# Kernel tuning notes

Hardware: AMD Instinct MI355X
Metric: run time of the kernel (lower is better)

## Reference

```python
import jax, jax.numpy as jnp
import numpy as np

B, T, D = 4096, 200, 64
H = 32  # hidden units of score MLP
NEG_INF = jnp.float32(-2**32 + 1)


def setup_inputs() -> dict:
    key = jax.random.key(0)
    k1, k2, k3, k4, k5 = jax.random.split(key, 5)
    query = jax.random.normal(k1, (B, 1, D), dtype=jnp.float32)
    keys = jax.random.normal(k2, (B, T, D), dtype=jnp.float32)
    mask = jax.random.randint(k3, (B, T), 0, 2) > 0
    mask = mask.at[:, 0].set(True)  # ensure at least one valid key per row
    # Glorot-normal-ish init for the tiny score MLP
    W1 = jax.random.normal(k4, (3 * D, H), dtype=jnp.float32) * jnp.sqrt(2.0 / (3 * D + H))
    b1 = jnp.zeros((H,), dtype=jnp.float32)
    W2 = jax.random.normal(k5, (H, 1), dtype=jnp.float32) * jnp.sqrt(2.0 / (H + 1))
    b2 = jnp.zeros((1,), dtype=jnp.float32)
    return {"query": query, "keys": keys, "mask": mask,
            "W1": W1, "b1": b1, "W2": W2, "b2": b2}


def reference(query, keys, mask, W1, b1, W2, b2):
    b, t, d = keys.shape
    q = jnp.broadcast_to(query, (b, t, d))            # tile query over seq
    att_in = jnp.concatenate([q, keys, q - keys], axis=-1)   # [B,T,3D]
    h = jax.nn.sigmoid(att_in @ W1 + b1)              # [B,T,H]
    score = (h @ W2 + b2)[..., 0]                     # [B,T]
    score = jnp.where(mask, score, NEG_INF)
    w = jax.nn.softmax(score, axis=-1)                # [B,T]
    out = jnp.einsum('bt,btd->bd', w, keys)           # weighted key sum
    return out[:, None, :]                            # [B,1,D]
```

## Files before the change

kernel.cpp:

```cpp
#include <hip/hip_runtime.h>
#include <hip/hip_bf16.h>


#define B 4096
#define T 200
#define D 64
#define H 32
#define LOG2E 1.44269504088896340736f
#define SOFF 16.0f
#define NTILE 13

typedef __attribute__((ext_vector_type(8))) short short8;
typedef __attribute__((ext_vector_type(4))) float f32x4;


__global__ __launch_bounds__(256) void prep_kernel(
        const float* __restrict__ W1,
        float*       __restrict__ ws)
{
    int n = blockIdx.x * 256 + threadIdx.x;
    if (blockIdx.x < 8) {
        int k = n >> 5;
        int j = n & 31;
        ws[n] = W1[k * H + j] + W1[(128 + k) * H + j];
    } else {
        int m = n - 2048;
        int e  = m & 7;
        int l  = (m >> 3) & 63;
        int fs = m >> 9;
        int ntile = fs >> 1, kstep = fs & 1;
        int k = kstep * 32 + (l >> 4) * 8 + e;
        int j = ntile * 16 + (l & 15);
        float v = W1[(64 + k) * H + j] - W1[(128 + k) * H + j];
        __hip_bfloat16 hv = __float2bfloat16(v);
        reinterpret_cast<unsigned short*>(ws + 2048)[m] =
            __builtin_bit_cast(unsigned short, hv);
    }
}

__device__ __forceinline__ unsigned short bf16u(float x) {
    __hip_bfloat16 h = __float2bfloat16(x);
    return __builtin_bit_cast(unsigned short, h);
}

__global__ __launch_bounds__(256) void attn_pool_kernel(
        const float* __restrict__ keys,
        const int*   __restrict__ mask,
        const unsigned short* __restrict__ wkf,
        const float* __restrict__ wsum,
        const float* __restrict__ b1,
        const float* __restrict__ W2,
        const float* __restrict__ query,
        float*       __restrict__ out)
{
    __shared__ float qsh[4][64];
    __shared__ float part[4][68];

    const int tid  = threadIdx.x;
    const int wv   = tid >> 6;
    const int lane = tid & 63;
    const int quad = lane >> 4;
    const int l15  = lane & 15;

    const int b    = blockIdx.x * 2 + (wv >> 1);
    const int half = wv & 1;

    qsh[wv][lane] = query[(size_t)b * D + lane];
    const int jq = lane & 31;
    const int kh = lane >> 5;
    float qac0 = kh ? 0.0f : b1[jq];
    float qac1 = 0.0f;
    #pragma unroll
    for (int k0 = 0; k0 < 32; k0 += 2) {
        int k = kh * 32 + k0;
        qac0 = fmaf(qsh[wv][k],     wsum[k * H + jq],       qac0);
        qac1 = fmaf(qsh[wv][k + 1], wsum[(k + 1) * H + jq], qac1);
    }
    float qac = qac0 + qac1;
    qac += __shfl_xor(qac, 32, 64);
    const float qa0 = __shfl(qac, l15, 64);
    const float qa1 = __shfl(qac, 16 + l15, 64);

    const short8* wf = reinterpret_cast<const short8*>(wkf);
    short8 bf0 = wf[0 * 64 + lane];
    short8 bf1 = wf[1 * 64 + lane];
    short8 bf2 = wf[2 * 64 + lane];
    short8 bf3 = wf[3 * 64 + lane];
    const float w20 = W2[l15];
    const float w21 = W2[16 + l15];

    const float4* krow = reinterpret_cast<const float4*>(keys + (size_t)b * (T * D));
    const int*    mrow = mask + (size_t)b * T;
    const int ib = quad * 2;

    float acc[16];
    #pragma unroll
    for (int j = 0; j < 16; ++j) acc[j] = 0.0f;
    float dacc = 0.0f;

    const int t0  = half * 7;
    const int ntl = half ? 6 : 7;

    float4 kA0 = krow[(t0 * 16 + l15) * 16 + ib + 0];
    float4 kA1 = krow[(t0 * 16 + l15) * 16 + ib + 1];
    float4 kA2 = krow[(t0 * 16 + l15) * 16 + 8 + ib + 0];
    float4 kA3 = krow[(t0 * 16 + l15) * 16 + 8 + ib + 1];
    int    mA  = mrow[t0 * 16 + l15];

    #pragma unroll 1
    for (int it = 0; it < ntl; ++it) {
        const int tile = t0 + it;
        float4 kB0 = kA0, kB1 = kA1, kB2 = kA2, kB3 = kA3;
        int    mB  = mA;
        if (it + 1 < ntl) {
            int tn  = (tile + 1) * 16 + l15;
            int trn = (tn < T) ? tn : (T - 1);
            kB0 = krow[trn * 16 + ib + 0];
            kB1 = krow[trn * 16 + ib + 1];
            kB2 = krow[trn * 16 + 8 + ib + 0];
            kB3 = krow[trn * 16 + 8 + ib + 1];
            mB  = mrow[trn];
        }

        short8 a0, a1;
        a0[0] = (short)bf16u(kA0.x); a0[1] = (short)bf16u(kA0.y);
        a0[2] = (short)bf16u(kA0.z); a0[3] = (short)bf16u(kA0.w);
        a0[4] = (short)bf16u(kA1.x); a0[5] = (short)bf16u(kA1.y);
        a0[6] = (short)bf16u(kA1.z); a0[7] = (short)bf16u(kA1.w);
        a1[0] = (short)bf16u(kA2.x); a1[1] = (short)bf16u(kA2.y);
        a1[2] = (short)bf16u(kA2.z); a1[3] = (short)bf16u(kA2.w);
        a1[4] = (short)bf16u(kA3.x); a1[5] = (short)bf16u(kA3.y);
        a1[6] = (short)bf16u(kA3.z); a1[7] = (short)bf16u(kA3.w);

        f32x4 c0 = {0.f, 0.f, 0.f, 0.f};
        f32x4 c1 = {0.f, 0.f, 0.f, 0.f};
        c0 = __builtin_amdgcn_mfma_f32_16x16x32_bf16(a0, bf0, c0, 0, 0, 0);
        c0 = __builtin_amdgcn_mfma_f32_16x16x32_bf16(a1, bf1, c0, 0, 0, 0);
        c1 = __builtin_amdgcn_mfma_f32_16x16x32_bf16(a0, bf2, c1, 0, 0, 0);
        c1 = __builtin_amdgcn_mfma_f32_16x16x32_bf16(a1, bf3, c1, 0, 0, 0);

        float p[4];
        #pragma unroll
        for (int r = 0; r < 4; ++r) {
            float x0 = c0[r] + qa0;
            float x1 = c1[r] + qa1;
            float s0 = __builtin_amdgcn_rcpf(1.0f + exp2f(-x0 * LOG2E));
            float s1 = __builtin_amdgcn_rcpf(1.0f + exp2f(-x1 * LOG2E));
            p[r] = fmaf(s0, w20, s1 * w21);
        }
        #pragma unroll
        for (int r = 0; r < 4; ++r) {
            #pragma unroll
            for (int off = 1; off <= 8; off <<= 1)
                p[r] += __shfl_xor(p[r], off, 64);
        }
        const int addr = (l15 >> 2) << 6;
        int q0 = __builtin_amdgcn_ds_bpermute(addr, __builtin_bit_cast(int, p[0]));
        int q1 = __builtin_amdgcn_ds_bpermute(addr, __builtin_bit_cast(int, p[1]));
        int q2 = __builtin_amdgcn_ds_bpermute(addr, __builtin_bit_cast(int, p[2]));
        int q3 = __builtin_amdgcn_ds_bpermute(addr, __builtin_bit_cast(int, p[3]));
        const int rsel = l15 & 3;
        int s01 = (rsel & 1) ? q1 : q0;
        int s23 = (rsel & 1) ? q3 : q2;
        float st = __builtin_bit_cast(float, (rsel & 2) ? s23 : s01);

        const int t = tile * 16 + l15;
        const float w = ((t < T) && (mA != 0)) ? exp2f((st - SOFF) * LOG2E) : 0.0f;

        acc[0]  = fmaf(w, kA0.x, acc[0]);  acc[1]  = fmaf(w, kA0.y, acc[1]);
        acc[2]  = fmaf(w, kA0.z, acc[2]);  acc[3]  = fmaf(w, kA0.w, acc[3]);
        acc[4]  = fmaf(w, kA1.x, acc[4]);  acc[5]  = fmaf(w, kA1.y, acc[5]);
        acc[6]  = fmaf(w, kA1.z, acc[6]);  acc[7]  = fmaf(w, kA1.w, acc[7]);
        acc[8]  = fmaf(w, kA2.x, acc[8]);  acc[9]  = fmaf(w, kA2.y, acc[9]);
        acc[10] = fmaf(w, kA2.z, acc[10]); acc[11] = fmaf(w, kA2.w, acc[11]);
        acc[12] = fmaf(w, kA3.x, acc[12]); acc[13] = fmaf(w, kA3.y, acc[13]);
        acc[14] = fmaf(w, kA3.z, acc[14]); acc[15] = fmaf(w, kA3.w, acc[15]);
        dacc += w;

        kA0 = kB0; kA1 = kB1; kA2 = kB2; kA3 = kB3; mA = mB;
    }

    #pragma unroll
    for (int j = 0; j < 16; ++j) {
        #pragma unroll
        for (int off = 1; off <= 8; off <<= 1)
            acc[j] += __shfl_xor(acc[j], off, 64);
    }
    #pragma unroll
    for (int off = 1; off <= 8; off <<= 1)
        dacc += __shfl_xor(dacc, off, 64);

    if (l15 == 0) {
        float4 o0 = {acc[0],  acc[1],  acc[2],  acc[3]};
        float4 o1 = {acc[4],  acc[5],  acc[6],  acc[7]};
        float4 o2 = {acc[8],  acc[9],  acc[10], acc[11]};
        float4 o3 = {acc[12], acc[13], acc[14], acc[15]};
        *reinterpret_cast<float4*>(&part[wv][quad * 8 + 0])      = o0;
        *reinterpret_cast<float4*>(&part[wv][quad * 8 + 4])      = o1;
        *reinterpret_cast<float4*>(&part[wv][32 + quad * 8 + 0]) = o2;
        *reinterpret_cast<float4*>(&part[wv][32 + quad * 8 + 4]) = o3;
    }
    if (lane == 0) part[wv][64] = dacc;
    __syncthreads();

    if (tid < 128) {
        int bb = tid >> 6;
        int d  = tid & 63;
        float s  = part[bb * 2][d]  + part[bb * 2 + 1][d];
        float dn = part[bb * 2][64] + part[bb * 2 + 1][64];
        out[((size_t)blockIdx.x * 2 + bb) * D + d] = s * __builtin_amdgcn_rcpf(dn);
    }
}

extern "C" void kernel_launch(void* const* d_in, const int* in_sizes, int n_in,
                              void* d_out, int out_size, void* d_ws, size_t ws_size,
                              hipStream_t stream) {
    const float* query = (const float*)d_in[0];
    const float* keys  = (const float*)d_in[1];
    const int*   mask  = (const int*)d_in[2];
    const float* W1    = (const float*)d_in[3];
    const float* b1    = (const float*)d_in[4];
    const float* W2    = (const float*)d_in[5];

    float* ws = (float*)d_ws;
    float* wsum = ws;
    unsigned short* wkf = (unsigned short*)(ws + 2048);

    prep_kernel<<<16, 256, 0, stream>>>(W1, ws);
    attn_pool_kernel<<<B / 2, 256, 0, stream>>>(keys, mask, wkf, wsum, b1, W2,
                                                query, (float*)d_out);
}
```

Before: 303.8 us.

## Assign one batch row per block, interleave tiles across four waves

Each block now handles a single batch row, and its four waves stride over the 13 key tiles round-robin. Before, each block handled two rows with two waves per row taking contiguous halves. This doubles the grid to B blocks and shortens each wave's serial loop, giving more latency hiding for the memory-bound key stream. Blocks are also remapped to batch rows with a stride of B/8, probably to spread concurrently running blocks across XCD/memory channels. The cost is more blocks, each redoing the query projection and weight-fragment loads, and a four-way reduction instead of a two-way one.

```diff
diff --git a/kernel.cpp b/kernel.cpp
--- a/kernel.cpp
+++ b/kernel.cpp
@@ -62,8 +62,7 @@
     const int quad = lane >> 4;
     const int l15  = lane & 15;
 
-    const int b    = blockIdx.x * 2 + (wv >> 1);
-    const int half = wv & 1;
+    const int b = (blockIdx.x & 7) * (B / 8) + (blockIdx.x >> 3);
 
     qsh[wv][lane] = query[(size_t)b * D + lane];
     const int jq = lane & 31;
@@ -98,22 +97,21 @@
     for (int j = 0; j < 16; ++j) acc[j] = 0.0f;
     float dacc = 0.0f;
 
-    const int t0  = half * 7;
-    const int ntl = half ? 6 : 7;
-
-    float4 kA0 = krow[(t0 * 16 + l15) * 16 + ib + 0];
-    float4 kA1 = krow[(t0 * 16 + l15) * 16 + ib + 1];
-    float4 kA2 = krow[(t0 * 16 + l15) * 16 + 8 + ib + 0];
-    float4 kA3 = krow[(t0 * 16 + l15) * 16 + 8 + ib + 1];
-    int    mA  = mrow[t0 * 16 + l15];
+    const int ntl = (wv == 0) ? 4 : 3;
+
+    float4 kA0 = krow[(wv * 16 + l15) * 16 + ib + 0];
+    float4 kA1 = krow[(wv * 16 + l15) * 16 + ib + 1];
+    float4 kA2 = krow[(wv * 16 + l15) * 16 + 8 + ib + 0];
+    float4 kA3 = krow[(wv * 16 + l15) * 16 + 8 + ib + 1];
+    int    mA  = mrow[wv * 16 + l15];
 
     #pragma unroll 1
     for (int it = 0; it < ntl; ++it) {
-        const int tile = t0 + it;
+        const int tile = wv + it * 4;
         float4 kB0 = kA0, kB1 = kA1, kB2 = kA2, kB3 = kA3;
         int    mB  = mA;
         if (it + 1 < ntl) {
-            int tn  = (tile + 1) * 16 + l15;
+            int tn  = (wv + (it + 1) * 4) * 16 + l15;
             int trn = (tn < T) ? tn : (T - 1);
             kB0 = krow[trn * 16 + ib + 0];
             kB1 = krow[trn * 16 + ib + 1];
@@ -203,12 +201,10 @@
     if (lane == 0) part[wv][64] = dacc;
     __syncthreads();
 
-    if (tid < 128) {
-        int bb = tid >> 6;
-        int d  = tid & 63;
-        float s  = part[bb * 2][d]  + part[bb * 2 + 1][d];
-        float dn = part[bb * 2][64] + part[bb * 2 + 1][64];
-        out[((size_t)blockIdx.x * 2 + bb) * D + d] = s * __builtin_amdgcn_rcpf(dn);
+    if (tid < 64) {
+        float s  = (part[0][tid] + part[1][tid]) + (part[2][tid] + part[3][tid]);
+        float dn = (part[0][64]  + part[1][64])  + (part[2][64]  + part[3][64]);
+        out[(size_t)b * D + tid] = s * __builtin_amdgcn_rcpf(dn);
     }
 }
 
@@ -227,6 +223,6 @@
     unsigned short* wkf = (unsigned short*)(ws + 2048);
 
     prep_kernel<<<16, 256, 0, stream>>>(W1, ws);
-    attn_pool_kernel<<<B / 2, 256, 0, stream>>>(keys, mask, wkf, wsum, b1, W2,
-                                                query, (float*)d_out);
-}
+    attn_pool_kernel<<<B, 256, 0, stream>>>(keys, mask, wkf, wsum, b1, W2,
+                                            query, (float*)d_out);
+}
```

Measured after the change: 301.3 us. Within noise of the previous version (-0.8%).
